# Performance work log

Hardware: AMD Instinct MI355X
Metric: run time of the kernel (lower is better)

The kernel has to match this reference:

```python
import jax, jax.numpy as jnp
import numpy as np

B, D, H = 4096, 1024, 1024


def setup_inputs() -> dict:
    key = jax.random.key(0)
    ks = jax.random.split(key, 20)
    s_in = 1.0 / np.sqrt(D)
    s_hid = 1.0 / np.sqrt(H)
    inp = {
        "x_t": jax.random.normal(ks[0], (B, D), dtype=jnp.float32),
        "h_t_1": jax.random.normal(ks[1], (B, H), dtype=jnp.float32),
        "c_t_1": jax.random.normal(ks[2], (B, H), dtype=jnp.float32),
        # input-to-hidden weights (nn.Linear: y = x @ W.T + b), stacked i,f,o,z
        "W": jax.random.uniform(ks[3], (4, H, D), minval=-s_in, maxval=s_in, dtype=jnp.float32),
        "bW": jax.random.uniform(ks[4], (4, H), minval=-s_in, maxval=s_in, dtype=jnp.float32),
        # hidden-to-hidden weights, stacked i,f,o,z
        "U": jax.random.uniform(ks[5], (4, H, H), minval=-s_hid, maxval=s_hid, dtype=jnp.float32),
        "bU": jax.random.uniform(ks[6], (4, H), minval=-s_hid, maxval=s_hid, dtype=jnp.float32),
    }
    return inp


def reference(x_t, h_t_1, c_t_1, W, bW, U, bU):
    # Two stacked GEMMs: [B,D]x[4,H,D] -> [4,B,H], [B,H]x[4,H,H] -> [4,B,H]
    gx = jnp.einsum("bd,ghd->gbh", x_t, W) + bW[:, None, :]
    gh = jnp.einsum("bh,gkh->gbk", h_t_1, U) + bU[:, None, :]
    g = gx + gh  # [4, B, H] pre-activations for i, f, o, z
    i = jax.nn.sigmoid(g[0])
    f = jax.nn.sigmoid(g[1])
    o = jax.nn.sigmoid(g[2])
    z = jnp.tanh(g[3])
    c_t = i * z + f * c_t_1
    h_t = o * jnp.tanh(c_t)
    return (h_t, c_t)
```

## Files before the change

### kernel.cpp

```cpp
#include <hip/hip_runtime.h>
#include <math.h>

#define Mm 4096
#define Nn 4096
#define Kk 2048

typedef __bf16 bf16x8 __attribute__((ext_vector_type(8)));
typedef float f32x4 __attribute__((ext_vector_type(4)));

__device__ __forceinline__ unsigned short f2bf(float f) {
    union { float f; unsigned u; } v; v.f = f;
    unsigned r = v.u + 0x7FFFu + ((v.u >> 16) & 1u);
    return (unsigned short)(r >> 16);
}

__device__ __forceinline__ float fast_tanh(float x) {
    return 1.f - 2.f / (1.f + __expf(2.f * x));
}

__global__ void pack_bf16(const float* __restrict__ x, const float* __restrict__ h,
                          const float* __restrict__ W, const float* __restrict__ U,
                          const float* __restrict__ bW, const float* __restrict__ bU,
                          unsigned short* __restrict__ Xc, unsigned short* __restrict__ Wc,
                          float* __restrict__ bsum) {
    if (blockIdx.x == 0) {
#pragma unroll
        for (int j = 0; j < 16; ++j) {
            int n = threadIdx.x * 16 + j;
            int hh = n >> 2, g = n & 3;
            bsum[n] = bW[g * 1024 + hh] + bU[g * 1024 + hh];
        }
    }
    const int PER = (4096 * 1024) / 4;
    for (int t = blockIdx.x * blockDim.x + threadIdx.x; t < 4 * PER;
         t += gridDim.x * blockDim.x) {
        int region = t >> 20;
        int i = t & (PER - 1);
        int row = i >> 8;
        int c4  = i & 255;
        const float* src = (region == 0) ? x : (region == 1) ? h : (region == 2) ? W : U;
        float4 v = reinterpret_cast<const float4*>(src)[i];
        ushort4 o;
        o.x = f2bf(v.x); o.y = f2bf(v.y); o.z = f2bf(v.z); o.w = f2bf(v.w);
        if (region < 2) {
            *reinterpret_cast<ushort4*>(Xc + (size_t)row * 2048 + (region << 10) + c4 * 4) = o;
        } else {
            int g = row >> 10, hh = row & 1023;
            int np = ((hh >> 4) << 6) + (g << 4) + (hh & 15);
            *reinterpret_cast<ushort4*>(Wc + (size_t)np * 2048 + ((region & 1) << 10) + c4 * 4) = o;
        }
    }
}

__device__ __forceinline__ void gl16(const void* g, void* l) {
    __builtin_amdgcn_global_load_lds(
        (const __attribute__((address_space(1))) void*)g,
        (__attribute__((address_space(3))) void*)l, 16, 0, 0);
}

__global__ __launch_bounds__(512, 2) void gemm_occ(const unsigned short* __restrict__ A,
                                                   const unsigned short* __restrict__ Bw,
                                                   const float* __restrict__ bsum,
                                                   const float* __restrict__ cprev,
                                                   float* __restrict__ out) {
    extern __shared__ char lds[];
    const int tid = threadIdx.x, lane = tid & 63, wave = tid >> 6;
    const int wm = wave >> 2, wn = wave & 3;

    const int bid = blockIdx.x;
    const int swz = (bid & 7) * 64 + (bid >> 3);
    const int bm = swz & 31, bn = swz >> 5;
    const size_t Crow0 = (size_t)bm * 128, Ccol0 = (size_t)bn * 256;

    {
    }
    const int sq = tid >> 3, ss = tid & 7;
    const int s2a = ss ^ (sq & 7);
    const char* aSrc = (const char*)A +
        (size_t)(Crow0 + sq + ((s2a >> 2) * 64)) * 4096 + (s2a & 3) * 16;
    const int bq0 = sq, bq1 = 64 + sq;
    const int s2b0 = ss ^ (bq0 & 7), s2b1 = ss ^ (bq1 & 7);
    const char* bSrc0 = (const char*)Bw +
        (size_t)(Ccol0 + bq0 + ((s2b0 >> 2) * 128)) * 4096 + (s2b0 & 3) * 16;
    const char* bSrc1 = (const char*)Bw +
        (size_t)(Ccol0 + bq1 + ((s2b1 >> 2) * 128)) * 4096 + (s2b1 & 3) * 16;

#define STGA(off, ktb) gl16(aSrc + (ktb), lds + (off) + wave * 1024)
#define STGB(off, ktb) do { \
        gl16(bSrc0 + (ktb), lds + (off) + wave * 1024); \
        gl16(bSrc1 + (ktb), lds + (off) + 8192 + wave * 1024); } while (0)

    const int aConst = (lane & 15) * 128 + (((wm * 4 + (lane >> 4)) ^ (lane & 7)) << 4);
    const int bConst = ((wn & 1) * 64 + (lane & 15)) * 128 +
                       ((((wn >> 1) * 4 + (lane >> 4)) ^ (lane & 7)) << 4);

#define LDAq(off, mf) (*(const bf16x8*)(lds + (off) + aConst + (mf) * 2048))
#define LDBq(off, nf) (*(const bf16x8*)(lds + (off) + bConst + (nf) * 2048))

    f32x4 acc[4][4] = {};
    bf16x8 af0, af1, af2, af3, bf0, bf1, bf2, bf3;

#define MFMA(a, b, c) __builtin_amdgcn_mfma_f32_16x16x32_bf16(a, b, c, 0, 0, 0)
#define CL16 \
    acc[0][0] = MFMA(af0, bf0, acc[0][0]); \
    acc[1][0] = MFMA(af1, bf0, acc[1][0]); \
    acc[2][0] = MFMA(af2, bf0, acc[2][0]); \
    acc[3][0] = MFMA(af3, bf0, acc[3][0]); \
    acc[0][1] = MFMA(af0, bf1, acc[0][1]); \
    acc[1][1] = MFMA(af1, bf1, acc[1][1]); \
    acc[2][1] = MFMA(af2, bf1, acc[2][1]); \
    acc[3][1] = MFMA(af3, bf1, acc[3][1]); \
    acc[0][2] = MFMA(af0, bf2, acc[0][2]); \
    acc[1][2] = MFMA(af1, bf2, acc[1][2]); \
    acc[2][2] = MFMA(af2, bf2, acc[2][2]); \
    acc[3][2] = MFMA(af3, bf2, acc[3][2]); \
    acc[0][3] = MFMA(af0, bf3, acc[0][3]); \
    acc[1][3] = MFMA(af1, bf3, acc[1][3]); \
    acc[2][3] = MFMA(af2, bf3, acc[2][3]); \
    acc[3][3] = MFMA(af3, bf3, acc[3][3]);

    STGA(0, 0);           STGB(24576, 0);
    STGA(8192, 64);       STGB(40960, 64);
    asm volatile("s_waitcnt vmcnt(3)" ::: "memory");
    __builtin_amdgcn_s_barrier();
    af0 = LDAq(0, 0); af1 = LDAq(0, 1); af2 = LDAq(0, 2); af3 = LDAq(0, 3);
    bf0 = LDBq(24576, 0); bf1 = LDBq(24576, 1); bf2 = LDBq(24576, 2); bf3 = LDBq(24576, 3);

    int oAr = 8192, oAs = 16384, oAx = 0;
    int oBr = 40960, oBs = 57344, oBx = 24576;

    for (int t = 0; t < 63; ++t) {
        const int kt2 = t + 2;
        const size_t ktb = (size_t)(kt2 <= 63 ? kt2 : 0) * 64;
        __builtin_amdgcn_s_setprio(1);
        CL16
        __builtin_amdgcn_s_setprio(0);
        STGA(oAs, ktb);
        STGB(oBs, ktb);
        asm volatile("s_waitcnt vmcnt(3)" ::: "memory");
        __builtin_amdgcn_s_barrier();
        af0 = LDAq(oAr, 0); af1 = LDAq(oAr, 1); af2 = LDAq(oAr, 2); af3 = LDAq(oAr, 3);
        bf0 = LDBq(oBr, 0); bf1 = LDBq(oBr, 1); bf2 = LDBq(oBr, 2); bf3 = LDBq(oBr, 3);
        int tA = oAx; oAx = oAr; oAr = oAs; oAs = tA;
        int tB = oBx; oBx = oBr; oBr = oBs; oBs = tB;
    }
    __builtin_amdgcn_s_setprio(1);
    CL16
    __builtin_amdgcn_s_setprio(0);

    const int hl = lane & 15;
    const int er0 = (lane >> 4) * 4;
    const int myh = (int)(Ccol0 >> 2) + wn * 16 + hl;
    const f32x4 bs = *(const f32x4*)(bsum + (size_t)myh * 4);

    float cp[4][4];
#pragma unroll
    for (int mf = 0; mf < 4; ++mf)
#pragma unroll
        for (int r = 0; r < 4; ++r)
            cp[mf][r] = cprev[(size_t)(Crow0 + wm * 64 + mf * 16 + er0 + r) * 1024 + myh];

#pragma unroll
    for (int mf = 0; mf < 4; ++mf)
#pragma unroll
        for (int r = 0; r < 4; ++r) {
            float gi = acc[mf][0][r] + bs[0];
            float gf = acc[mf][1][r] + bs[1];
            float go = acc[mf][2][r] + bs[2];
            float gz = acc[mf][3][r] + bs[3];
            float iv = 1.f / (1.f + __expf(-gi));
            float fv = 1.f / (1.f + __expf(-gf));
            float ov = 1.f / (1.f + __expf(-go));
            float zv = fast_tanh(gz);
            float cc = fmaf(iv, zv, fv * cp[mf][r]);
            float hv = ov * fast_tanh(cc);
            const size_t oidx =
                (size_t)(Crow0 + wm * 64 + mf * 16 + er0 + r) * 1024 + myh;
            out[oidx] = hv;
            out[(1 << 22) + oidx] = cc;
        }

    asm volatile("s_waitcnt vmcnt(0)" ::: "memory");
}

extern "C" void kernel_launch(void* const* d_in, const int* in_sizes, int n_in,
                              void* d_out, int out_size, void* d_ws, size_t ws_size,
                              hipStream_t stream) {
    const float* x  = (const float*)d_in[0];
    const float* h  = (const float*)d_in[1];
    const float* c  = (const float*)d_in[2];
    const float* W  = (const float*)d_in[3];
    const float* bW = (const float*)d_in[4];
    const float* U  = (const float*)d_in[5];
    const float* bU = (const float*)d_in[6];
    float* out = (float*)d_out;

    char* ws = (char*)d_ws;
    unsigned short* Xc = (unsigned short*)ws;
    unsigned short* Wc = (unsigned short*)(ws + ((size_t)16 << 20));
    float* bsum = (float*)(ws + ((size_t)32 << 20));

    (void)hipFuncSetAttribute((const void*)gemm_occ,
                              hipFuncAttributeMaxDynamicSharedMemorySize, 73728);

    hipLaunchKernelGGL(pack_bf16, dim3(2048), dim3(256), 0, stream,
                       x, h, W, U, bW, bU, Xc, Wc, bsum);
    hipLaunchKernelGGL(gemm_occ, dim3(512), dim3(512), 73728, stream,
                       Xc, Wc, bsum, c, out);
}
```

Measured before the change: 96.43 us.

## Use 256x256 tiles with 16 waves and a 128-wide K double-buffered pipeline

Replaces the 128x256 tile, 8-wave GEMM with a 256x256 tile run by 1024-thread blocks (16 waves), 128-element K steps, and a two-stage LDS double buffer of 128KB. The main loop is split into four sub-phases per K step that interleave A-fragment LDS reads, MFMA clusters, and global-to-LDS prefetches separated by barriers and sched_barriers. The larger tile raises arithmetic intensity and halves the grid to 256 blocks, but it needs 128KB of LDS per block, which limits occupancy to one block per CU. It also adds more barriers per K step.

```diff
diff --git a/kernel.cpp b/kernel.cpp
--- a/kernel.cpp
+++ b/kernel.cpp
@@ -58,95 +58,136 @@
         (__attribute__((address_space(3))) void*)l, 16, 0, 0);
 }
 
-__global__ __launch_bounds__(512, 2) void gemm_occ(const unsigned short* __restrict__ A,
-                                                   const unsigned short* __restrict__ Bw,
-                                                   const float* __restrict__ bsum,
-                                                   const float* __restrict__ cprev,
-                                                   float* __restrict__ out) {
+__global__ __launch_bounds__(1024, 4) void gemm_w16(const unsigned short* __restrict__ A,
+                                                    const unsigned short* __restrict__ Bw,
+                                                    const float* __restrict__ bsum,
+                                                    const float* __restrict__ cprev,
+                                                    float* __restrict__ out) {
     extern __shared__ char lds[];
     const int tid = threadIdx.x, lane = tid & 63, wave = tid >> 6;
     const int wm = wave >> 2, wn = wave & 3;
+    const int ahh = wm >> 1, bhb = wn >> 1;
 
     const int bid = blockIdx.x;
-    const int swz = (bid & 7) * 64 + (bid >> 3);
-    const int bm = swz & 31, bn = swz >> 5;
-    const size_t Crow0 = (size_t)bm * 128, Ccol0 = (size_t)bn * 256;
-
-    {
-    }
-    const int sq = tid >> 3, ss = tid & 7;
-    const int s2a = ss ^ (sq & 7);
-    const char* aSrc = (const char*)A +
-        (size_t)(Crow0 + sq + ((s2a >> 2) * 64)) * 4096 + (s2a & 3) * 16;
-    const int bq0 = sq, bq1 = 64 + sq;
-    const int s2b0 = ss ^ (bq0 & 7), s2b1 = ss ^ (bq1 & 7);
-    const char* bSrc0 = (const char*)Bw +
-        (size_t)(Ccol0 + bq0 + ((s2b0 >> 2) * 128)) * 4096 + (s2b0 & 3) * 16;
-    const char* bSrc1 = (const char*)Bw +
-        (size_t)(Ccol0 + bq1 + ((s2b1 >> 2) * 128)) * 4096 + (s2b1 & 3) * 16;
-
-#define STGA(off, ktb) gl16(aSrc + (ktb), lds + (off) + wave * 1024)
-#define STGB(off, ktb) do { \
-        gl16(bSrc0 + (ktb), lds + (off) + wave * 1024); \
-        gl16(bSrc1 + (ktb), lds + (off) + 8192 + wave * 1024); } while (0)
-
-    const int aConst = (lane & 15) * 128 + (((wm * 4 + (lane >> 4)) ^ (lane & 7)) << 4);
-    const int bConst = ((wn & 1) * 64 + (lane & 15)) * 128 +
-                       ((((wn >> 1) * 4 + (lane >> 4)) ^ (lane & 7)) << 4);
-
-#define LDAq(off, mf) (*(const bf16x8*)(lds + (off) + aConst + (mf) * 2048))
-#define LDBq(off, nf) (*(const bf16x8*)(lds + (off) + bConst + (nf) * 2048))
+    const int swz = (bid & 7) * 32 + (bid >> 3);
+    const int bm = swz & 15, bn = swz >> 4;
+    const size_t Crow0 = (size_t)bm * 256, Ccol0 = (size_t)bn * 256;
+
+    const int q = tid >> 3, s = tid & 7;
+    const int s2 = s ^ (q & 7);
+    const char* aSrc[2];
+    const char* bSrc[2];
+#pragma unroll
+    for (int ah = 0; ah < 2; ++ah) {
+        aSrc[ah] = (const char*)A  + (size_t)(Crow0 + ah * 128 + q) * 4096 + (s2 << 4);
+        bSrc[ah] = (const char*)Bw + (size_t)(Ccol0 + ah * 128 + q) * 4096 + (s2 << 4);
+    }
+
+#define STG_A(p, ah, kb) gl16(aSrc[ah] + (kb), lds + ((p) * 2 + (ah)) * 16384 + tid * 16)
+#define STG_B(p, hb, kb) gl16(bSrc[hb] + (kb), lds + 65536 + ((p) * 2 + (hb)) * 16384 + tid * 16)
+
+    const int arowB = ((wm & 1) * 64 + (lane & 15)) * 128;
+    const int browB = ((wn & 1) * 64 + (lane & 15)) * 128;
+    const int c0 = (((lane >> 4) << 4)) ^ ((lane & 7) << 4);
+    const int c1 = (64 + ((lane >> 4) << 4)) ^ ((lane & 7) << 4);
+
+#define LDAm(p, mf, ck) (*(const bf16x8*)(lds + ((p) * 2 + ahh) * 16384 + arowB + (mf) * 2048 + (ck)))
+#define LDBm(p, nf, ck) (*(const bf16x8*)(lds + 65536 + ((p) * 2 + bhb) * 16384 + browB + (nf) * 2048 + (ck)))
 
     f32x4 acc[4][4] = {};
-    bf16x8 af0, af1, af2, af3, bf0, bf1, bf2, bf3;
+    bf16x8 b00, b01, b10, b11, b20, b21, b30, b31;
+    bf16x8 ac0, ac1, an0, an1;
 
 #define MFMA(a, b, c) __builtin_amdgcn_mfma_f32_16x16x32_bf16(a, b, c, 0, 0, 0)
-#define CL16 \
-    acc[0][0] = MFMA(af0, bf0, acc[0][0]); \
-    acc[1][0] = MFMA(af1, bf0, acc[1][0]); \
-    acc[2][0] = MFMA(af2, bf0, acc[2][0]); \
-    acc[3][0] = MFMA(af3, bf0, acc[3][0]); \
-    acc[0][1] = MFMA(af0, bf1, acc[0][1]); \
-    acc[1][1] = MFMA(af1, bf1, acc[1][1]); \
-    acc[2][1] = MFMA(af2, bf1, acc[2][1]); \
-    acc[3][1] = MFMA(af3, bf1, acc[3][1]); \
-    acc[0][2] = MFMA(af0, bf2, acc[0][2]); \
-    acc[1][2] = MFMA(af1, bf2, acc[1][2]); \
-    acc[2][2] = MFMA(af2, bf2, acc[2][2]); \
-    acc[3][2] = MFMA(af3, bf2, acc[3][2]); \
-    acc[0][3] = MFMA(af0, bf3, acc[0][3]); \
-    acc[1][3] = MFMA(af1, bf3, acc[1][3]); \
-    acc[2][3] = MFMA(af2, bf3, acc[2][3]); \
-    acc[3][3] = MFMA(af3, bf3, acc[3][3]);
-
-    STGA(0, 0);           STGB(24576, 0);
-    STGA(8192, 64);       STGB(40960, 64);
-    asm volatile("s_waitcnt vmcnt(3)" ::: "memory");
+#define CL8(mf, A0_, A1_) \
+    acc[mf][0] = MFMA(A0_, b00, acc[mf][0]); \
+    acc[mf][1] = MFMA(A0_, b10, acc[mf][1]); \
+    acc[mf][2] = MFMA(A0_, b20, acc[mf][2]); \
+    acc[mf][3] = MFMA(A0_, b30, acc[mf][3]); \
+    acc[mf][0] = MFMA(A1_, b01, acc[mf][0]); \
+    acc[mf][1] = MFMA(A1_, b11, acc[mf][1]); \
+    acc[mf][2] = MFMA(A1_, b21, acc[mf][2]); \
+    acc[mf][3] = MFMA(A1_, b31, acc[mf][3]);
+
+#define SGB0 __builtin_amdgcn_sched_barrier(0)
+#define SBAR __builtin_amdgcn_s_barrier()
+
+#define GROUP_FULL(p, kb2) \
+    { \
+         \
+        an0 = LDAm(p, 1, c0); an1 = LDAm(p, 1, c1); \
+        SGB0; \
+        __builtin_amdgcn_s_setprio(1); CL8(0, ac0, ac1) __builtin_amdgcn_s_setprio(0); \
+        SBAR; \
+         \
+        ac0 = LDAm(p, 2, c0); ac1 = LDAm(p, 2, c1); \
+        SGB0; \
+        __builtin_amdgcn_s_setprio(1); CL8(1, an0, an1) __builtin_amdgcn_s_setprio(0); \
+        STG_B(p, 0, kb2); \
+        SBAR; \
+         \
+        an0 = LDAm(p, 3, c0); an1 = LDAm(p, 3, c1); \
+        SGB0; \
+        __builtin_amdgcn_s_setprio(1); CL8(2, ac0, ac1) __builtin_amdgcn_s_setprio(0); \
+        STG_B(p, 1, kb2); \
+        asm volatile("s_waitcnt vmcnt(2)" ::: "memory"); \
+        SBAR; \
+         \
+        ac0 = LDAm((p) ^ 1, 0, c0); ac1 = LDAm((p) ^ 1, 0, c1); \
+        SGB0; \
+        __builtin_amdgcn_s_setprio(1); CL8(3, an0, an1) __builtin_amdgcn_s_setprio(0); \
+        b00 = LDBm((p) ^ 1, 0, c0); b01 = LDBm((p) ^ 1, 0, c1); \
+        b10 = LDBm((p) ^ 1, 1, c0); b11 = LDBm((p) ^ 1, 1, c1); \
+        b20 = LDBm((p) ^ 1, 2, c0); b21 = LDBm((p) ^ 1, 2, c1); \
+        b30 = LDBm((p) ^ 1, 3, c0); b31 = LDBm((p) ^ 1, 3, c1); \
+        STG_A(p, 0, kb2); STG_A(p, 1, kb2); \
+        SBAR; \
+    }
+
+#define GROUP_TAIL(p) \
+    { \
+        an0 = LDAm(p, 1, c0); an1 = LDAm(p, 1, c1); \
+        SGB0; \
+        __builtin_amdgcn_s_setprio(1); CL8(0, ac0, ac1) __builtin_amdgcn_s_setprio(0); \
+        SBAR; \
+        ac0 = LDAm(p, 2, c0); ac1 = LDAm(p, 2, c1); \
+        SGB0; \
+        __builtin_amdgcn_s_setprio(1); CL8(1, an0, an1) __builtin_amdgcn_s_setprio(0); \
+        SBAR; \
+        an0 = LDAm(p, 3, c0); an1 = LDAm(p, 3, c1); \
+        SGB0; \
+        __builtin_amdgcn_s_setprio(1); CL8(2, ac0, ac1) __builtin_amdgcn_s_setprio(0); \
+        asm volatile("s_waitcnt vmcnt(0)" ::: "memory"); \
+        SBAR; \
+        ac0 = LDAm((p) ^ 1, 0, c0); ac1 = LDAm((p) ^ 1, 0, c1); \
+        SGB0; \
+        __builtin_amdgcn_s_setprio(1); CL8(3, an0, an1) __builtin_amdgcn_s_setprio(0); \
+        b00 = LDBm((p) ^ 1, 0, c0); b01 = LDBm((p) ^ 1, 0, c1); \
+        b10 = LDBm((p) ^ 1, 1, c0); b11 = LDBm((p) ^ 1, 1, c1); \
+        b20 = LDBm((p) ^ 1, 2, c0); b21 = LDBm((p) ^ 1, 2, c1); \
+        b30 = LDBm((p) ^ 1, 3, c0); b31 = LDBm((p) ^ 1, 3, c1); \
+        SBAR; \
+    }
+
+    STG_B(0, 0, 0); STG_B(0, 1, 0); STG_A(0, 0, 0); STG_A(0, 1, 0);
+    STG_B(1, 0, 128); STG_B(1, 1, 128); STG_A(1, 0, 128); STG_A(1, 1, 128);
+    asm volatile("s_waitcnt vmcnt(4)" ::: "memory");
     __builtin_amdgcn_s_barrier();
-    af0 = LDAq(0, 0); af1 = LDAq(0, 1); af2 = LDAq(0, 2); af3 = LDAq(0, 3);
-    bf0 = LDBq(24576, 0); bf1 = LDBq(24576, 1); bf2 = LDBq(24576, 2); bf3 = LDBq(24576, 3);
-
-    int oAr = 8192, oAs = 16384, oAx = 0;
-    int oBr = 40960, oBs = 57344, oBx = 24576;
-
-    for (int t = 0; t < 63; ++t) {
-        const int kt2 = t + 2;
-        const size_t ktb = (size_t)(kt2 <= 63 ? kt2 : 0) * 64;
-        __builtin_amdgcn_s_setprio(1);
-        CL16
-        __builtin_amdgcn_s_setprio(0);
-        STGA(oAs, ktb);
-        STGB(oBs, ktb);
-        asm volatile("s_waitcnt vmcnt(3)" ::: "memory");
-        __builtin_amdgcn_s_barrier();
-        af0 = LDAq(oAr, 0); af1 = LDAq(oAr, 1); af2 = LDAq(oAr, 2); af3 = LDAq(oAr, 3);
-        bf0 = LDBq(oBr, 0); bf1 = LDBq(oBr, 1); bf2 = LDBq(oBr, 2); bf3 = LDBq(oBr, 3);
-        int tA = oAx; oAx = oAr; oAr = oAs; oAs = tA;
-        int tB = oBx; oBx = oBr; oBr = oBs; oBs = tB;
-    }
-    __builtin_amdgcn_s_setprio(1);
-    CL16
-    __builtin_amdgcn_s_setprio(0);
+    b00 = LDBm(0, 0, c0); b01 = LDBm(0, 0, c1);
+    b10 = LDBm(0, 1, c0); b11 = LDBm(0, 1, c1);
+    b20 = LDBm(0, 2, c0); b21 = LDBm(0, 2, c1);
+    b30 = LDBm(0, 3, c0); b31 = LDBm(0, 3, c1);
+    ac0 = LDAm(0, 0, c0); ac1 = LDAm(0, 0, c1);
+
+    for (int it = 0; it < 15; ++it) {
+        const int t0 = 2 * it;
+        const size_t kb2a = (size_t)(t0 + 2) * 128;
+        const size_t kb2b = (size_t)(t0 + 3) * 128;
+        GROUP_FULL(0, kb2a)
+        GROUP_FULL(1, kb2b)
+    }
+    GROUP_TAIL(0)
+    GROUP_TAIL(1)
 
     const int hl = lane & 15;
     const int er0 = (lane >> 4) * 4;
@@ -200,11 +241,11 @@
     unsigned short* Wc = (unsigned short*)(ws + ((size_t)16 << 20));
     float* bsum = (float*)(ws + ((size_t)32 << 20));
 
-    (void)hipFuncSetAttribute((const void*)gemm_occ,
-                              hipFuncAttributeMaxDynamicSharedMemorySize, 73728);
+    (void)hipFuncSetAttribute((const void*)gemm_w16,
+                              hipFuncAttributeMaxDynamicSharedMemorySize, 131072);
 
     hipLaunchKernelGGL(pack_bf16, dim3(2048), dim3(256), 0, stream,
                        x, h, W, U, bW, bU, Xc, Wc, bsum);
-    hipLaunchKernelGGL(gemm_occ, dim3(512), dim3(512), 73728, stream,
+    hipLaunchKernelGGL(gemm_w16, dim3(256), dim3(1024), 131072, stream,
                        Xc, Wc, bsum, c, out);
 }
```

After: 86.44 us. 1.12x faster.
